# Performance work log

Hardware: AMD Instinct MI355X
Metric: run time of the kernel (lower is better)

Reference implementation:

```python
import jax, jax.numpy as jnp
import numpy as np

BS, N, NEIGHBOR_NUM, SUPPORT = 8, 2048, 20, 7
K0, C1, C2 = 32, 64, 256  # conv_0 kernel_num, conv_1 out, conv_2 out (local_latent_size)
NUM_STRUCT = 16
LOCAL_RATE = 2048 // (8 * NUM_STRUCT)  # 16


def gather_neighbors(t, idx):
    # t: (b, v, d), idx: (b, v, n) -> (b, v, n, d)
    return jax.vmap(lambda a, i: a[i])(t, idx)


def knn_index(vertices, k):
    # (b, v, 3) -> (b, v, k) indices of k nearest neighbors (excluding self)
    inner = jnp.einsum('bid,bjd->bij', vertices, vertices)
    q = jnp.sum(vertices * vertices, axis=-1)
    dist = -2.0 * inner + q[:, :, None] + q[:, None, :]
    idx = jax.lax.top_k(-dist, k + 1)[1]  # smallest distances
    return idx[:, :, 1:]


def operator3d(neighbor_index, vertices, weights, displacement, support_num, kernel_num):
    b, v, n = neighbor_index.shape
    neigh = gather_neighbors(vertices, neighbor_index)  # (b,v,n,3)
    disp = neigh - vertices[:, :, None, :]
    theta = jax.nn.relu(disp @ displacement)            # (b,v,n,s*k)
    theta = theta.reshape(b, v, n, support_num, kernel_num)
    theta = jnp.max(theta, axis=2) * weights            # (b,v,s,k)
    return jnp.sum(theta, axis=2)                       # (b,v,k)


def operator_nd(neighbor_index, vertices, feature_map, weights, bias, displacement,
                support_num, out_channel):
    b, v, n = neighbor_index.shape
    neigh = gather_neighbors(vertices, neighbor_index)
    disp = neigh - vertices[:, :, None, :]
    theta = jax.nn.relu(disp @ displacement)            # (b,v,n,s*oc)
    feat = feature_map @ weights + bias                 # (b,v,(s+1)*oc)
    feat_center = feat[:, :, :out_channel]
    feat_support = feat[:, :, out_channel:]
    feat_support = gather_neighbors(feat_support, neighbor_index)  # (b,v,n,s*oc)
    act = (theta * feat_support).reshape(b, v, n, support_num, out_channel)
    act = jnp.sum(jnp.max(act, axis=2), axis=2)         # (b,v,oc)
    return feat_center + act


def pooling(vertices, feature_map, pooling_rate, neighbor_num, seed):
    b, v, _ = vertices.shape
    idx = knn_index(vertices, neighbor_num)
    pooled = jnp.max(gather_neighbors(feature_map, idx), axis=2)
    pool_num = v // pooling_rate
    sample_idx = np.random.default_rng(seed).permutation(v)[:pool_num]
    sample_idx = jnp.asarray(sample_idx)
    return vertices[:, sample_idx, :], pooled[:, sample_idx, :]


def setup_inputs() -> dict:
    key = jax.random.key(0)
    ks = jax.random.split(key, 9)
    vertices = jax.random.normal(ks[0], (BS, N, 3), dtype=jnp.float32)

    def unif(k, shape, stdv):
        return jax.random.uniform(k, shape, minval=-stdv, maxval=stdv, dtype=jnp.float32)

    s0 = 1.0 / np.sqrt(SUPPORT * K0)
    s1 = 1.0 / np.sqrt(C1 * (SUPPORT + 1))
    s2 = 1.0 / np.sqrt(C2 * (SUPPORT + 1))
    return {
        'vertices': vertices,
        'w0_weights': unif(ks[1], (1, 1, SUPPORT, K0), s0),
        'w0_disp': unif(ks[2], (3, SUPPORT * K0), s0),
        'w1_weights': unif(ks[3], (K0, (SUPPORT + 1) * C1), s1),
        'w1_bias': unif(ks[4], ((SUPPORT + 1) * C1,), s1),
        'w1_disp': unif(ks[5], (3, SUPPORT * C1), s1),
        'w2_weights': unif(ks[6], (C1, (SUPPORT + 1) * C2), s2),
        'w2_bias': unif(ks[7], ((SUPPORT + 1) * C2,), s2),
        'w2_disp': unif(ks[8], (3, SUPPORT * C2), s2),
    }


def reference(vertices, w0_weights, w0_disp, w1_weights, w1_bias, w1_disp,
              w2_weights, w2_bias, w2_disp):
    ni = knn_index(vertices, NEIGHBOR_NUM)
    fm0 = operator3d(ni, vertices, w0_weights, w0_disp, SUPPORT, K0)
    fm0 = jax.nn.relu(fm0)  # dropout in eval mode = identity
    fm1 = jax.nn.relu(operator_nd(ni, vertices, fm0, w1_weights, w1_bias, w1_disp, SUPPORT, C1))
    v1, fm1 = pooling(vertices, fm1, pooling_rate=8, neighbor_num=8, seed=1)
    ni2 = knn_index(v1, NEIGHBOR_NUM)
    fm2 = jax.nn.relu(operator_nd(ni2, v1, fm1, w2_weights, w2_bias, w2_disp, SUPPORT, C2))
    v2, fm3 = pooling(v1, fm2, pooling_rate=LOCAL_RATE, neighbor_num=LOCAL_RATE, seed=2)
    return v2, fm3
```

## Files before the change

### kernel.cpp

```cpp
#include <hip/hip_runtime.h>
#include <hip/hip_bf16.h>
#include <stdint.h>
#include <string.h>

#define NB   8
#define NV   2048
#define NN   20
#define SUP  7
#define K0   32
#define C1   64
#define C2   256
#define NV2  256
#define NP2  16
#define COLL_CAP 320

typedef unsigned __int128 u128;

struct CPcg { u128 state; u128 inc; bool has32; uint32_t cached; };

constexpr u128 PCG_MULT = (((u128)2549297995355413924ULL) << 64) | 4865540595714422341ULL;

constexpr uint64_t c_rotr64(uint64_t v, unsigned r) {
    return (v >> (r & 63u)) | (v << ((64u - r) & 63u));
}
constexpr uint64_t pcg_next64(CPcg& g) {
    g.state = g.state * PCG_MULT + g.inc;
    uint64_t hi = (uint64_t)(g.state >> 64);
    uint64_t lo = (uint64_t)g.state;
    return c_rotr64(hi ^ lo, (unsigned)(hi >> 58));
}
constexpr uint32_t pcg_next32(CPcg& g) {
    if (g.has32) { g.has32 = false; return g.cached; }
    uint64_t n = pcg_next64(g);
    g.has32 = true;
    g.cached = (uint32_t)(n >> 32);
    return (uint32_t)n;
}
constexpr uint64_t rand_interval(CPcg& g, uint64_t mx) {
    if (mx == 0) return 0;
    uint64_t mask = mx;
    mask |= mask >> 1; mask |= mask >> 2; mask |= mask >> 4;
    mask |= mask >> 8; mask |= mask >> 16; mask |= mask >> 32;
    uint64_t v = 0;
    while ((v = ((uint64_t)pcg_next32(g) & mask)) > mx) {
    }
    return v;
}
constexpr uint32_t hashmix(uint32_t value, uint32_t& hc) {
    value ^= hc; hc *= 0x931e8875u; value *= hc; value ^= value >> 16; return value;
}
constexpr uint32_t mixpool(uint32_t x, uint32_t y) {
    uint32_t r = (x * 0xca01f9ddu) - (y * 0x4973f715u);
    r ^= r >> 16; return r;
}
constexpr CPcg make_rng(uint32_t entropy) {
    uint32_t pool[4] = {0, 0, 0, 0};
    uint32_t hc = 0x43b0d7e5u;
    for (int i = 0; i < 4; i++) {
        uint32_t v = (i == 0) ? entropy : 0u;
        pool[i] = hashmix(v, hc);
    }
    for (int isrc = 0; isrc < 4; isrc++)
        for (int idst = 0; idst < 4; idst++)
            if (isrc != idst) pool[idst] = mixpool(pool[idst], hashmix(pool[isrc], hc));
    uint32_t w[8] = {};
    uint32_t hb = 0x8b51f9ddu;
    for (int i = 0; i < 8; i++) {
        uint32_t dv = pool[i & 3];
        dv ^= hb; hb *= 0x58f38dedu; dv *= hb; dv ^= dv >> 16; w[i] = dv;
    }
    uint64_t sd[4] = {};
    for (int k = 0; k < 4; k++) sd[k] = (uint64_t)w[2 * k] | ((uint64_t)w[2 * k + 1] << 32);
    u128 s = (((u128)sd[0]) << 64) | sd[1];
    u128 iq = (((u128)sd[2]) << 64) | sd[3];
    CPcg g{};
    g.state = 0;
    g.inc = (iq << 1) | 1;
    g.state = g.state * PCG_MULT + g.inc;
    g.state += s;
    g.state = g.state * PCG_MULT + g.inc;
    g.has32 = false; g.cached = 0;
    return g;
}

struct PermOut { int p1[256]; int p2[16]; };

constexpr PermOut compute_perms() {
    PermOut o{};
    {
        CPcg g = make_rng(1u);
        int arr[2048] = {};
        for (int i = 0; i < 2048; i++) arr[i] = i;
        for (int i = 2047; i >= 1; i--) {
            int j = (int)rand_interval(g, (uint64_t)i);
            int t = arr[i]; arr[i] = arr[j]; arr[j] = t;
        }
        for (int i = 0; i < 256; i++) o.p1[i] = arr[i];
    }
    {
        CPcg g = make_rng(2u);
        int arr[256] = {};
        for (int i = 0; i < 256; i++) arr[i] = i;
        for (int i = 255; i >= 1; i--) {
            int j = (int)rand_interval(g, (uint64_t)i);
            int t = arr[i]; arr[i] = arr[j]; arr[j] = t;
        }
        for (int i = 0; i < 16; i++) o.p2[i] = arr[i];
    }
    return o;
}

struct PermArg1 { int v[256]; };
struct PermArg2 { int v[16]; };

__global__ __launch_bounds__(384) void v2_kernel(const float* __restrict__ verts,
                                                 float* __restrict__ out,
                                                 PermArg2 cidx) {
    int t = threadIdx.x;
    if (t < NB * NP2 * 3) {
        int b = t / (NP2 * 3);
        int rem = t - b * (NP2 * 3);
        int j = rem / 3;
        int c = rem - j * 3;
        out[t] = verts[(b * NV + cidx.v[j]) * 3 + c];
    }
}

template<int N, int CPL>
__global__ __launch_bounds__(256, 4) void knn_coop_kernel(const float* __restrict__ verts,
                                                          int* __restrict__ nbr) {
    __shared__ float4 svq[N];
    __shared__ int hist[256];
    __shared__ unsigned long long coll[COLL_CAP];
    __shared__ int cnt;
    __shared__ unsigned wred[8];

    constexpr int RPB = 4;
    int bpb = N / RPB;
    int b = blockIdx.x / bpb;
    int rbase = (blockIdx.x % bpb) * RPB;
    const float* vb = verts + (size_t)b * N * 3;

    for (int t = threadIdx.x; t < N; t += 256) {
        float x = vb[t * 3 + 0], y = vb[t * 3 + 1], z = vb[t * 3 + 2];
        svq[t] = make_float4(x, y, z, x * x + y * y + z * z);
    }
    __syncthreads();

    int wid = threadIdx.x >> 6, lane = threadIdx.x & 63;

    for (int rr = 0; rr < RPB; rr++) {
        int i = rbase + rr;
        float4 vi = svq[i];
        float vx = vi.x, vy = vi.y, vz = vi.z;
        float qi = vi.w;

        hist[threadIdx.x] = 0;
        if (threadIdx.x == 0) cnt = 0;
        __syncthreads();

        unsigned key[CPL];
        unsigned lmin = 0xFFFFFFFFu, lmax = 0u;
        #pragma unroll
        for (int t = 0; t < CPL; t++) {
            int j = wid * (CPL * 64) + t * 64 + lane;
            float4 vj = svq[j];
            float inner = vx * vj.x + vy * vj.y + vz * vj.z;
            float dist = (-2.0f * inner + qi) + vj.w;
            unsigned u = __float_as_uint(dist);
            u = (u & 0x80000000u) ? ~u : (u | 0x80000000u);
            if (j == i) u = 0xFFFFFFFFu;
            key[t] = u;
            if (u != 0xFFFFFFFFu) {
                lmin = (u < lmin) ? u : lmin;
                lmax = (u > lmax) ? u : lmax;
            }
        }
        #pragma unroll
        for (int off = 32; off >= 1; off >>= 1) {
            unsigned o1 = (unsigned)__shfl_xor((int)lmin, off);
            unsigned o2 = (unsigned)__shfl_xor((int)lmax, off);
            lmin = (o1 < lmin) ? o1 : lmin;
            lmax = (o2 > lmax) ? o2 : lmax;
        }
        if (lane == 0) { wred[wid] = lmin; wred[4 + wid] = lmax; }
        __syncthreads();
        lmin = wred[0];
        lmax = wred[4];
        #pragma unroll
        for (int w = 1; w < 4; w++) {
            lmin = (wred[w] < lmin) ? wred[w] : lmin;
            lmax = (wred[4 + w] > lmax) ? wred[4 + w] : lmax;
        }
        float scale = (lmax > lmin) ? 255.0f / (float)(lmax - lmin) : 0.0f;

        #pragma unroll
        for (int t = 0; t < CPL; t++) {
            int bi = (key[t] == 0xFFFFFFFFu) ? 255
                     : (int)((float)(key[t] - lmin) * scale);
            bi = (bi > 255) ? 255 : bi;
            atomicAdd(&hist[bi], 1);
        }
        __syncthreads();

        int h0 = hist[lane * 4 + 0];
        int h1 = hist[lane * 4 + 1];
        int h2 = hist[lane * 4 + 2];
        int h3 = hist[lane * 4 + 3];
        int s = h0 + h1 + h2 + h3;
        int cum = s;
        #pragma unroll
        for (int off = 1; off < 64; off <<= 1) {
            int v = __shfl_up(cum, off);
            if (lane >= off) cum += v;
        }
        unsigned long long bal = __ballot(cum >= NN);
        int L = __ffsll((long long)bal) - 1;
        int baseL = __shfl(cum, L) - __shfl(s, L);
        int g0 = __shfl(h0, L), g1 = __shfl(h1, L), g2 = __shfl(h2, L);
        int B;
        if (baseL + g0 >= NN)            B = 4 * L + 0;
        else if (baseL + g0 + g1 >= NN)  B = 4 * L + 1;
        else if (baseL + g0 + g1 + g2 >= NN) B = 4 * L + 2;
        else                              B = 4 * L + 3;

        #pragma unroll
        for (int t = 0; t < CPL; t++) {
            int bi = (key[t] == 0xFFFFFFFFu) ? 255
                     : (int)((float)(key[t] - lmin) * scale);
            bi = (bi > 255) ? 255 : bi;
            if (bi <= B) {
                int pos = atomicAdd(&cnt, 1);
                if (pos < COLL_CAP) {
                    int j = wid * (CPL * 64) + t * 64 + lane;
                    coll[pos] = ((unsigned long long)key[t] << 32) | (unsigned)j;
                }
            }
        }
        __syncthreads();
        int count = cnt;
        if (count > COLL_CAP) count = COLL_CAP;

        int* dst = nbr + ((size_t)b * N + i) * NN;
        for (int e = threadIdx.x; e < count; e += 256) {
            unsigned long long me = coll[e];
            int rank = 0;
            for (int m = 0; m < count; m++) rank += (coll[m] < me);
            if (rank < NN) dst[rank] = (int)(me & 0xFFFFFFFFull);
        }
        __syncthreads();
    }
}

__global__ __launch_bounds__(256) void op3d_kernel(const float* __restrict__ verts,
                                                   const int* __restrict__ nbr,
                                                   const float* __restrict__ w0w,
                                                   const float* __restrict__ w0d,
                                                   float* __restrict__ fm0) {
    __shared__ float swd[3 * SUP * K0];
    __shared__ float sww[SUP * K0];
    for (int t = threadIdx.x; t < 3 * SUP * K0; t += 256) swd[t] = w0d[t];
    for (int t = threadIdx.x; t < SUP * K0; t += 256) sww[t] = w0w[t];
    __syncthreads();

    int gid = blockIdx.x * 256 + threadIdx.x;
    int b = gid >> 11, v = gid & (NV - 1);
    const float* vb = verts + b * NV * 3;
    float vx = vb[v * 3], vy = vb[v * 3 + 1], vz = vb[v * 3 + 2];

    const int* nb = nbr + gid * NN;
    float dx[NN], dy[NN], dz[NN];
    #pragma unroll
    for (int n = 0; n < NN; n++) {
        int j = nb[n];
        dx[n] = vb[j * 3 + 0] - vx;
        dy[n] = vb[j * 3 + 1] - vy;
        dz[n] = vb[j * 3 + 2] - vz;
    }
    float* out = fm0 + gid * K0;
    #pragma unroll 1
    for (int k = 0; k < K0; k++) {
        float acc = 0.f;
        #pragma unroll
        for (int s = 0; s < SUP; s++) {
            float w0 = swd[0 * 224 + s * K0 + k];
            float w1 = swd[1 * 224 + s * K0 + k];
            float w2 = swd[2 * 224 + s * K0 + k];
            float m = 0.f;
            #pragma unroll
            for (int n = 0; n < NN; n++) {
                float t = dx[n] * w0 + dy[n] * w1 + dz[n] * w2;
                t = fmaxf(t, 0.f);
                m = fmaxf(m, t);
            }
            acc += m * sww[s * K0 + k];
        }
        out[k] = fmaxf(acc, 0.f);
    }
}

template<int K, int N>
__global__ __launch_bounds__(256) void feat_gemm(const float* __restrict__ fm,
                                                 const float* __restrict__ w,
                                                 const float* __restrict__ bias,
                                                 float* __restrict__ feat) {
    __shared__ float sf[64][K];
    __shared__ float swt[K][64];
    int cb = blockIdx.x % (N / 64), rb = blockIdx.x / (N / 64);
    int r0 = rb * 64, c0 = cb * 64;

    for (int t = threadIdx.x; t < 64 * K; t += 256)
        sf[t / K][t % K] = fm[(size_t)(r0 + t / K) * K + (t % K)];
    for (int t = threadIdx.x; t < K * 64; t += 256)
        swt[t >> 6][t & 63] = w[(size_t)(t >> 6) * N + c0 + (t & 63)];
    __syncthreads();

    int col = threadIdx.x & 63, rg = threadIdx.x >> 6;
    float bv = bias[c0 + col];
    float acc[16];
    #pragma unroll
    for (int r = 0; r < 16; r++) acc[r] = bv;
    #pragma unroll 1
    for (int k = 0; k < K; k++) {
        float wk = swt[k][col];
        #pragma unroll
        for (int r = 0; r < 16; r++) acc[r] += sf[rg * 16 + r][k] * wk;
    }
    #pragma unroll
    for (int r = 0; r < 16; r++)
        feat[(size_t)(r0 + rg * 16 + r) * N + c0 + col] = acc[r];
}

__global__ __launch_bounds__(256) void opnd1_gather(const float* __restrict__ verts,
                                                    const int* __restrict__ nbr,
                                                    const float* __restrict__ feat1,
                                                    const float* __restrict__ w1d,
                                                    float* __restrict__ fm1) {
    __shared__ float swd[3 * SUP * C1];
    for (int t = threadIdx.x; t < 3 * SUP * C1; t += 256) swd[t] = w1d[t];
    __syncthreads();

    int wid = threadIdx.x >> 6, lane = threadIdx.x & 63;
    int b = blockIdx.x & 7;
    int vtx = b * NV + (blockIdx.x >> 3) * 4 + wid;
    int v = vtx & (NV - 1);
    const float* vb = verts + b * NV * 3;
    const int* nb = nbr + vtx * NN;
    float vx = vb[v * 3], vy = vb[v * 3 + 1], vz = vb[v * 3 + 2];

    float w0r[SUP], w1r[SUP], w2r[SUP];
    #pragma unroll
    for (int ss = 0; ss < SUP; ss++) {
        w0r[ss] = swd[0 * (SUP * C1) + ss * C1 + lane];
        w1r[ss] = swd[1 * (SUP * C1) + ss * C1 + lane];
        w2r[ss] = swd[2 * (SUP * C1) + ss * C1 + lane];
    }

    const float* fb = feat1 + (size_t)b * NV * (8 * C1);
    float m[SUP];
    #pragma unroll
    for (int ss = 0; ss < SUP; ss++) m[ss] = -3.4e38f;

    #pragma unroll 4
    for (int n = 0; n < NN; n++) {
        int j = nb[n];
        float dx = vb[j * 3 + 0] - vx;
        float dy = vb[j * 3 + 1] - vy;
        float dz = vb[j * 3 + 2] - vz;
        const float* row = fb + (size_t)j * (8 * C1) + C1 + lane;
        #pragma unroll
        for (int ss = 0; ss < SUP; ss++) {
            float th = fmaxf(dx * w0r[ss] + dy * w1r[ss] + dz * w2r[ss], 0.f);
            m[ss] = fmaxf(m[ss], th * row[ss * C1]);
        }
    }
    float fcen = fb[(size_t)v * (8 * C1) + lane];
    float total = 0.f;
    #pragma unroll
    for (int ss = 0; ss < SUP; ss++) total += m[ss];
    fm1[vtx * C1 + lane] = fmaxf(fcen + total, 0.f);
}

__global__ __launch_bounds__(256) void opnd2_gather(const float* __restrict__ v1,
                                                    const int* __restrict__ nbr2,
                                                    const float* __restrict__ feat2,
                                                    const float* __restrict__ w2d,
                                                    float* __restrict__ fm2) {
    __shared__ float swd[3 * SUP * C2];
    for (int t = threadIdx.x; t < 3 * SUP * C2; t += 256) swd[t] = w2d[t];
    __syncthreads();

    int jj = threadIdx.x >> 6, lane = threadIdx.x & 63;
    int b = blockIdx.x & 7;
    int v = blockIdx.x >> 3;
    int vtx = b * NV2 + v;
    const float* vb = v1 + b * NV2 * 3;
    const int* nb = nbr2 + vtx * NN;
    float vx = vb[v * 3], vy = vb[v * 3 + 1], vz = vb[v * 3 + 2];

    int cj = jj * 64 + lane;
    float w0r[SUP], w1r[SUP], w2r[SUP];
    #pragma unroll
    for (int ss = 0; ss < SUP; ss++) {
        w0r[ss] = swd[0 * (SUP * C2) + ss * C2 + cj];
        w1r[ss] = swd[1 * (SUP * C2) + ss * C2 + cj];
        w2r[ss] = swd[2 * (SUP * C2) + ss * C2 + cj];
    }
    const float* fb = feat2 + (size_t)b * NV2 * (8 * C2);

    float m[SUP];
    #pragma unroll
    for (int ss = 0; ss < SUP; ss++) m[ss] = -3.4e38f;

    #pragma unroll 4
    for (int n = 0; n < NN; n++) {
        int j = nb[n];
        float dx = vb[j * 3 + 0] - vx;
        float dy = vb[j * 3 + 1] - vy;
        float dz = vb[j * 3 + 2] - vz;
        const float* row = fb + (size_t)j * (8 * C2) + C2 + cj;
        #pragma unroll
        for (int ss = 0; ss < SUP; ss++) {
            float th = fmaxf(dx * w0r[ss] + dy * w1r[ss] + dz * w2r[ss], 0.f);
            m[ss] = fmaxf(m[ss], th * row[ss * C2]);
        }
    }
    float total = 0.f;
    #pragma unroll
    for (int ss = 0; ss < SUP; ss++) total += m[ss];
    float fcen = fb[(size_t)v * (8 * C2) + cj];
    fm2[(size_t)vtx * C2 + cj] = fmaxf(fcen + total, 0.f);
}

__global__ __launch_bounds__(256) void pool1_kernel(const float* __restrict__ verts,
                                                    const int* __restrict__ nbr1,
                                                    const float* __restrict__ fm1,
                                                    float* __restrict__ v1,
                                                    float* __restrict__ fm1p,
                                                    PermArg1 pa) {
    int wid = threadIdx.x >> 6, lane = threadIdx.x & 63;
    int gid = blockIdx.x * 4 + wid;
    int b = gid >> 8, p = gid & 255;
    int sv = pa.v[p];
    const int* nb = nbr1 + (b * NV + sv) * NN;
    float m = -3.4e38f;
    #pragma unroll
    for (int n = 0; n < 8; n++) {
        m = fmaxf(m, fm1[(b * NV + nb[n]) * C1 + lane]);
    }
    fm1p[gid * C1 + lane] = m;
    if (lane < 3) v1[gid * 3 + lane] = verts[(b * NV + sv) * 3 + lane];
}

__global__ __launch_bounds__(256) void pool2_kernel(const int* __restrict__ nbr2,
                                                    const float* __restrict__ fm2,
                                                    float* __restrict__ out,
                                                    PermArg2 pa) {
    int wid = threadIdx.x >> 6, lane = threadIdx.x & 63;
    int gid = blockIdx.x * 4 + wid;
    int b = gid >> 4, p = gid & 15;
    int sv = pa.v[p];
    const int* nb = nbr2 + (b * NV2 + sv) * NN;
    #pragma unroll 1
    for (int jj = 0; jj < 4; jj++) {
        int c = lane + jj * 64;
        float m = -3.4e38f;
        #pragma unroll
        for (int n = 0; n < 16; n++) {
            m = fmaxf(m, fm2[(b * NV2 + nb[n]) * C2 + c]);
        }
        out[NB * NP2 * 3 + gid * C2 + c] = m;
    }
}

extern "C" void kernel_launch(void* const* d_in, const int* in_sizes, int n_in,
                              void* d_out, int out_size, void* d_ws, size_t ws_size,
                              hipStream_t stream) {
    (void)in_sizes; (void)n_in; (void)out_size; (void)ws_size;
    const float* verts = (const float*)d_in[0];
    const float* w0w = (const float*)d_in[1];
    const float* w0d = (const float*)d_in[2];
    const float* w1w = (const float*)d_in[3];
    const float* w1b = (const float*)d_in[4];
    const float* w1d = (const float*)d_in[5];
    const float* w2w = (const float*)d_in[6];
    const float* w2b = (const float*)d_in[7];
    const float* w2d = (const float*)d_in[8];
    float* out = (float*)d_out;

    static const PermOut perms = compute_perms();

    PermArg1 pa1;
    PermArg2 pa2, pac;
    memcpy(pa1.v, perms.p1, sizeof(pa1.v));
    memcpy(pa2.v, perms.p2, sizeof(pa2.v));
    for (int j = 0; j < 16; j++) pac.v[j] = perms.p1[perms.p2[j]];

    char* ws = (char*)d_ws;
    size_t off = 0;
    auto alloc = [&](size_t bytes) -> void* {
        void* p = ws + off;
        off += (bytes + 255) & ~(size_t)255;
        return p;
    };
    int*   nbr1  = (int*)  alloc((size_t)NB * NV * NN * 4);
    float* fm0   = (float*)alloc((size_t)NB * NV * K0 * 4);
    float* feat1 = (float*)alloc((size_t)NB * NV * 8 * C1 * 4);
    float* fm1   = (float*)alloc((size_t)NB * NV * C1 * 4);
    float* v1    = (float*)alloc((size_t)NB * NV2 * 3 * 4);
    float* fm1p  = (float*)alloc((size_t)NB * NV2 * C1 * 4);
    int*   nbr2  = (int*)  alloc((size_t)NB * NV2 * NN * 4);
    float* feat2 = (float*)alloc((size_t)NB * NV2 * 8 * C2 * 4);
    float* fm2   = (float*)alloc((size_t)NB * NV2 * C2 * 4);

    v2_kernel<<<1, 384, 0, stream>>>(verts, out, pac);
    knn_coop_kernel<NV, NV / 256><<<NB * (NV / 4), 256, 0, stream>>>(verts, nbr1);
    op3d_kernel<<<64, 256, 0, stream>>>(verts, nbr1, w0w, w0d, fm0);
    feat_gemm<K0, 8 * C1><<<(NB * NV / 64) * (8 * C1 / 64), 256, 0, stream>>>(fm0, w1w, w1b, feat1);
    opnd1_gather<<<NB * NV / 4, 256, 0, stream>>>(verts, nbr1, feat1, w1d, fm1);
    pool1_kernel<<<NB * NV2 / 4, 256, 0, stream>>>(verts, nbr1, fm1, v1, fm1p, pa1);
    knn_coop_kernel<NV2, NV2 / 256><<<NB * (NV2 / 4), 256, 0, stream>>>(v1, nbr2);
    feat_gemm<C1, 8 * C2><<<(NB * NV2 / 64) * (8 * C2 / 64), 256, 0, stream>>>(fm1p, w2w, w2b, feat2);
    opnd2_gather<<<NB * NV2, 256, 0, stream>>>(v1, nbr2, feat2, w2d, fm2);
    pool2_kernel<<<32, 256, 0, stream>>>(nbr2, fm2, out, pa2);
}
```

Before: 239.5 us.

## Split kNN block into two wave-pair groups processing separate query rows

The kNN kernel now splits each 256-thread block into two groups of two wavefronts. Each group handles its own query rows with private histogram, collection buffer, counter and min/max reduction slots. Each wave now scans twice as many candidates per row. The change halves the number of blocks, drops the per-row sync after histogram zeroing and the trailing sync, and aims for more work per wave and less block-wide synchronisation per row. In exchange, each wave carries more registers, and the rank sort uses only 128 threads per row.

Result: faster. 221.1 us (-7.7%).

```diff
diff --git a/kernel.cpp b/kernel.cpp
--- a/kernel.cpp
+++ b/kernel.cpp
@@ -127,20 +127,20 @@
 }
 
 template<int N, int CPL>
-__global__ __launch_bounds__(256, 4) void knn_coop_kernel(const float* __restrict__ verts,
+__global__ __launch_bounds__(256, 4) void knn_pair_kernel(const float* __restrict__ verts,
                                                           int* __restrict__ nbr) {
     __shared__ float4 svq[N];
-    __shared__ int hist[256];
-    __shared__ unsigned long long coll[COLL_CAP];
-    __shared__ int cnt;
-    __shared__ unsigned wred[8];
-
-    constexpr int RPB = 4;
-    int bpb = N / RPB;
+    __shared__ int hist[2][256];
+    __shared__ unsigned long long coll[2][COLL_CAP];
+    __shared__ int cnt[2];
+    __shared__ unsigned wred[2][4];
+
+    constexpr int RPG = 4;
+    int bpb = N / (2 * RPG);
     int b = blockIdx.x / bpb;
-    int rbase = (blockIdx.x % bpb) * RPB;
+    int rbase = (blockIdx.x % bpb) * (2 * RPG);
+
     const float* vb = verts + (size_t)b * N * 3;
-
     for (int t = threadIdx.x; t < N; t += 256) {
         float x = vb[t * 3 + 0], y = vb[t * 3 + 1], z = vb[t * 3 + 2];
         svq[t] = make_float4(x, y, z, x * x + y * y + z * z);
@@ -148,22 +148,27 @@
     __syncthreads();
 
     int wid = threadIdx.x >> 6, lane = threadIdx.x & 63;
-
-    for (int rr = 0; rr < RPB; rr++) {
-        int i = rbase + rr;
+    int g = wid >> 1;
+    int wg = wid & 1;
+    int tig = threadIdx.x & 127;
+    int* myhist = hist[g];
+    unsigned long long* mycoll = coll[g];
+
+    for (int rr = 0; rr < RPG; rr++) {
+        int i = rbase + g * RPG + rr;
         float4 vi = svq[i];
         float vx = vi.x, vy = vi.y, vz = vi.z;
         float qi = vi.w;
 
-        hist[threadIdx.x] = 0;
-        if (threadIdx.x == 0) cnt = 0;
-        __syncthreads();
+        myhist[tig * 2 + 0] = 0;
+        myhist[tig * 2 + 1] = 0;
+        if (tig == 0) cnt[g] = 0;
 
         unsigned key[CPL];
         unsigned lmin = 0xFFFFFFFFu, lmax = 0u;
         #pragma unroll
         for (int t = 0; t < CPL; t++) {
-            int j = wid * (CPL * 64) + t * 64 + lane;
+            int j = wg * (CPL * 64) + t * 64 + lane;
             float4 vj = svq[j];
             float inner = vx * vj.x + vy * vj.y + vz * vj.z;
             float dist = (-2.0f * inner + qi) + vj.w;
@@ -183,15 +188,11 @@
             lmin = (o1 < lmin) ? o1 : lmin;
             lmax = (o2 > lmax) ? o2 : lmax;
         }
-        if (lane == 0) { wred[wid] = lmin; wred[4 + wid] = lmax; }
+        if (lane == 0) { wred[g][wg] = lmin; wred[g][2 + wg] = lmax; }
         __syncthreads();
-        lmin = wred[0];
-        lmax = wred[4];
-        #pragma unroll
-        for (int w = 1; w < 4; w++) {
-            lmin = (wred[w] < lmin) ? wred[w] : lmin;
-            lmax = (wred[4 + w] > lmax) ? wred[4 + w] : lmax;
-        }
+
+        lmin = (wred[g][0] < wred[g][1]) ? wred[g][0] : wred[g][1];
+        lmax = (wred[g][2] > wred[g][3]) ? wred[g][2] : wred[g][3];
         float scale = (lmax > lmin) ? 255.0f / (float)(lmax - lmin) : 0.0f;
 
         #pragma unroll
@@ -199,14 +200,14 @@
             int bi = (key[t] == 0xFFFFFFFFu) ? 255
                      : (int)((float)(key[t] - lmin) * scale);
             bi = (bi > 255) ? 255 : bi;
-            atomicAdd(&hist[bi], 1);
+            atomicAdd(&myhist[bi], 1);
         }
         __syncthreads();
 
-        int h0 = hist[lane * 4 + 0];
-        int h1 = hist[lane * 4 + 1];
-        int h2 = hist[lane * 4 + 2];
-        int h3 = hist[lane * 4 + 3];
+        int h0 = myhist[lane * 4 + 0];
+        int h1 = myhist[lane * 4 + 1];
+        int h2 = myhist[lane * 4 + 2];
+        int h3 = myhist[lane * 4 + 3];
         int s = h0 + h1 + h2 + h3;
         int cum = s;
         #pragma unroll
@@ -230,25 +231,24 @@
                      : (int)((float)(key[t] - lmin) * scale);
             bi = (bi > 255) ? 255 : bi;
             if (bi <= B) {
-                int pos = atomicAdd(&cnt, 1);
+                int pos = atomicAdd(&cnt[g], 1);
                 if (pos < COLL_CAP) {
-                    int j = wid * (CPL * 64) + t * 64 + lane;
-                    coll[pos] = ((unsigned long long)key[t] << 32) | (unsigned)j;
+                    int j = wg * (CPL * 64) + t * 64 + lane;
+                    mycoll[pos] = ((unsigned long long)key[t] << 32) | (unsigned)j;
                 }
             }
         }
         __syncthreads();
-        int count = cnt;
+        int count = cnt[g];
         if (count > COLL_CAP) count = COLL_CAP;
 
         int* dst = nbr + ((size_t)b * N + i) * NN;
-        for (int e = threadIdx.x; e < count; e += 256) {
-            unsigned long long me = coll[e];
+        for (int e = tig; e < count; e += 128) {
+            unsigned long long me = mycoll[e];
             int rank = 0;
-            for (int m = 0; m < count; m++) rank += (coll[m] < me);
+            for (int m = 0; m < count; m++) rank += (mycoll[m] < me);
             if (rank < NN) dst[rank] = (int)(me & 0xFFFFFFFFull);
         }
-        __syncthreads();
     }
 }
 
@@ -514,12 +514,12 @@
     float* fm2   = (float*)alloc((size_t)NB * NV2 * C2 * 4);
 
     v2_kernel<<<1, 384, 0, stream>>>(verts, out, pac);
-    knn_coop_kernel<NV, NV / 256><<<NB * (NV / 4), 256, 0, stream>>>(verts, nbr1);
+    knn_pair_kernel<NV, NV / 128><<<NB * (NV / 8), 256, 0, stream>>>(verts, nbr1);
     op3d_kernel<<<64, 256, 0, stream>>>(verts, nbr1, w0w, w0d, fm0);
     feat_gemm<K0, 8 * C1><<<(NB * NV / 64) * (8 * C1 / 64), 256, 0, stream>>>(fm0, w1w, w1b, feat1);
     opnd1_gather<<<NB * NV / 4, 256, 0, stream>>>(verts, nbr1, feat1, w1d, fm1);
     pool1_kernel<<<NB * NV2 / 4, 256, 0, stream>>>(verts, nbr1, fm1, v1, fm1p, pa1);
-    knn_coop_kernel<NV2, NV2 / 256><<<NB * (NV2 / 4), 256, 0, stream>>>(v1, nbr2);
+    knn_pair_kernel<NV2, NV2 / 128><<<NB * (NV2 / 8), 256, 0, stream>>>(v1, nbr2);
     feat_gemm<C1, 8 * C2><<<(NB * NV2 / 64) * (8 * C2 / 64), 256, 0, stream>>>(fm1p, w2w, w2b, feat2);
     opnd2_gather<<<NB * NV2, 256, 0, stream>>>(v1, nbr2, feat2, w2d, fm2);
     pool2_kernel<<<32, 256, 0, stream>>>(nbr2, fm2, out, pa2);
```
